# Performance work log

Hardware: AMD Instinct MI355X
Metric: run time of the kernel (lower is better)

Reference implementation:

```python
import jax, jax.numpy as jnp
import numpy as np

HEADS = 4
HIDDEN = 128
NEG_SLOPE = 0.2
BN_EPS = 1e-5


def setup_inputs() -> dict:
    key = jax.random.key(0)
    ks = jax.random.split(key, 10)
    N, E, C, H = 10000, 320000, HIDDEN, HEADS
    D = C  # out_channels per head == hidden_channels
    glorot = lambda k, shape, fan: jax.random.normal(k, shape, dtype=jnp.float32) * np.float32(np.sqrt(2.0 / fan))
    x = jax.random.normal(ks[0], (N, C), dtype=jnp.float32)
    edge_index = jax.random.randint(ks[1], (2, E), 0, N, dtype=jnp.int64)
    W_l = glorot(ks[2], (C, H * D), C + H * D)
    b_l = jnp.zeros((H * D,), dtype=jnp.float32)
    W_r = glorot(ks[3], (C, H * D), C + H * D)
    b_r = jnp.zeros((H * D,), dtype=jnp.float32)
    att = glorot(ks[4], (H, D), D)
    bias = jnp.zeros((D,), dtype=jnp.float32)
    gamma = jnp.ones((D,), dtype=jnp.float32)
    beta = jnp.zeros((D,), dtype=jnp.float32)
    return {"x": x, "edge_index": edge_index, "W_l": W_l, "b_l": b_l,
            "W_r": W_r, "b_r": b_r, "att": att, "bias": bias,
            "gamma": gamma, "beta": beta}


def reference(x, edge_index, W_l, b_l, W_r, b_r, att, bias, gamma, beta):
    N, C = x.shape
    H = HEADS
    D = C
    # add self loops (PyG default add_self_loops=True)
    loops = jnp.arange(N, dtype=edge_index.dtype)
    src = jnp.concatenate([edge_index[0], loops])  # [E+N]
    dst = jnp.concatenate([edge_index[1], loops])  # [E+N]
    # GATv2: separate source/target transforms (share_weights=False)
    xl = (x @ W_l + b_l).reshape(N, H, D)  # source-side features
    xr = (x @ W_r + b_r).reshape(N, H, D)  # target-side features
    # per-edge score: a^T LeakyReLU(xl_j + xr_i)
    m = jax.nn.leaky_relu(xl[src] + xr[dst], negative_slope=NEG_SLOPE)  # [E',H,D]
    e = jnp.einsum('ehd,hd->eh', m, att)  # [E',H]
    # segment softmax over destination nodes
    emax = jax.ops.segment_max(e, dst, num_segments=N)  # [N,H]
    ee = jnp.exp(e - emax[dst])
    denom = jax.ops.segment_sum(ee, dst, num_segments=N)  # [N,H]
    alpha = ee / (denom[dst] + 1e-16)  # [E',H]
    # aggregate: sum_j alpha_ij * xl_j
    out = jax.ops.segment_sum(alpha[..., None] * xl[src], dst, num_segments=N)  # [N,H,D]
    out = out.mean(axis=1) + bias  # concat=False -> mean over heads, then bias
    # BatchNorm1d (training-mode batch statistics) + ReLU; dropout p=0
    mu = out.mean(axis=0)
    var = out.var(axis=0)
    out = gamma * (out - mu) * jax.lax.rsqrt(var + BN_EPS) + beta
    return jax.nn.relu(out)
```

## Files before the change

kernel.cpp:

```cpp
#include <hip/hip_runtime.h>
#include <math.h>

#define HEADS 4
#define HD 512
#define NEG 0.2f
#define CAP 96
#define BNB 64

typedef __attribute__((ext_vector_type(8))) short bf16x8;
typedef __attribute__((ext_vector_type(4))) float f32x4;

__device__ __forceinline__ unsigned short f2b(float f) {
    unsigned u = __float_as_uint(f);
    unsigned r = (u + 0x7fff + ((u >> 16) & 1)) >> 16;
    return (unsigned short)r;
}
__device__ __forceinline__ unsigned pack2(float a, float b) {
    return (unsigned)f2b(a) | ((unsigned)f2b(b) << 16);
}
__device__ __forceinline__ float lo16(unsigned u) { return __uint_as_float(u << 16); }
__device__ __forceinline__ float hi16(unsigned u) { return __uint_as_float(u & 0xffff0000u); }

template<int CTRL>
__device__ __forceinline__ float dpp_mov(float v) {
    int x = __builtin_amdgcn_mov_dpp(__float_as_int(v), CTRL, 0xF, 0xF, true);
    return __int_as_float(x);
}
__device__ __forceinline__ float rowsum16(float s) {
    s += dpp_mov<0xB1>(s);
    s += dpp_mov<0x4E>(s);
    s += dpp_mov<0x124>(s);
    s += dpp_mov<0x128>(s);
    return s;
}

__global__ __launch_bounds__(256) void prologue1(
    const float* __restrict__ Wl, const float* __restrict__ Wr,
    unsigned short* __restrict__ wlt, unsigned short* __restrict__ wrt,
    const float* __restrict__ x, unsigned short* __restrict__ xb, int n8,
    const int* __restrict__ ei, int E, int* __restrict__ deg,
    int* __restrict__ adjf, int cvtxBlocks)
{
    const int bid = blockIdx.x;
    const int tid = threadIdx.x;
    if (bid < 128) {
        __shared__ float t[32][33];
        const int bx = bid & 15, by = (bid >> 4) & 3, bz = bid >> 6;
        const float* W = bz ? Wr : Wl;
        unsigned short* Wt = bz ? wrt : wlt;
        const int c0 = bx * 32, k0 = by * 32;
        {
            int k = tid >> 3, c4 = (tid & 7) * 4;
            float4 v = *(const float4*)(W + (size_t)(k0 + k) * 512 + c0 + c4);
            t[k][c4] = v.x; t[k][c4 + 1] = v.y; t[k][c4 + 2] = v.z; t[k][c4 + 3] = v.w;
        }
        __syncthreads();
        {
            int c = tid >> 3, k4 = (tid & 7) * 4;
            ushort4 o;
            o.x = f2b(t[k4][c]); o.y = f2b(t[k4 + 1][c]);
            o.z = f2b(t[k4 + 2][c]); o.w = f2b(t[k4 + 3][c]);
            *(ushort4*)(Wt + (size_t)(c0 + c) * 128 + k0 + k4) = o;
        }
    } else if (bid < 128 + cvtxBlocks) {
        int i = (bid - 128) * 256 + tid;
        if (i < n8) {
            const float4* px = (const float4*)(x + (size_t)i * 8);
            float4 f0 = px[0], f1 = px[1];
            uint4 u;
            u.x = pack2(f0.x, f0.y); u.y = pack2(f0.z, f0.w);
            u.z = pack2(f1.x, f1.y); u.w = pack2(f1.z, f1.w);
            ((uint4*)xb)[i] = u;
        }
    } else {
        int e = (bid - 128 - cvtxBlocks) * 256 + tid;
        if (e < E) {
            int src = ei[e], dst = ei[E + e];
            int pos = atomicAdd(&deg[dst], 1);
            if (pos < CAP) adjf[(size_t)dst * CAP + pos] = src;
        }
    }
}

__global__ __launch_bounds__(256) void prologue2(
    const unsigned short* __restrict__ xb,
    const unsigned short* __restrict__ wlt, const unsigned short* __restrict__ wrt,
    const float* __restrict__ bl, const float* __restrict__ br,
    unsigned short* __restrict__ xlb, unsigned short* __restrict__ xrb, int N)
{
    __shared__ float tile[4][16][132];

    const int bx = blockIdx.x, by = blockIdx.y;
    const int wv = threadIdx.x >> 6;
    const int lane = threadIdx.x & 63;
    const int wsel = by >> 2;
    const int cb0 = (by & 3) * 128;
    const unsigned short* Wt = wsel ? wrt : wlt;
    const float* bias = wsel ? br : bl;
    unsigned short* out = wsel ? xrb : xlb;

    const int r0 = bx * 64 + wv * 16;
    const int row16 = lane & 15;
    const int kg = lane >> 4;
    int ar = r0 + row16;
    int arc = (ar < N) ? ar : (N - 1);
    const unsigned short* xrow = xb + (size_t)arc * 128;

    f32x4 acc[8];
    #pragma unroll
    for (int i = 0; i < 8; ++i) acc[i] = (f32x4){0.f, 0.f, 0.f, 0.f};

    #pragma unroll
    for (int ks = 0; ks < 4; ++ks) {
        bf16x8 a = *(const bf16x8*)(xrow + ks * 32 + kg * 8);
        #pragma unroll
        for (int cb = 0; cb < 8; ++cb) {
            int col = cb0 + cb * 16 + row16;
            bf16x8 b = *(const bf16x8*)(Wt + (size_t)col * 128 + ks * 32 + kg * 8);
            acc[cb] = __builtin_amdgcn_mfma_f32_16x16x32_bf16(a, b, acc[cb], 0, 0, 0);
        }
    }

    #pragma unroll
    for (int cb = 0; cb < 8; ++cb) {
        int c = cb * 16 + row16;
        #pragma unroll
        for (int r = 0; r < 4; ++r)
            tile[wv][kg * 4 + r][c] = acc[cb][r];
    }
    __syncthreads();

    #pragma unroll
    for (int p = 0; p < 4; ++p) {
        int row = p * 4 + (lane >> 4);
        int grow = r0 + row;
        if (grow < N) {
            int c8 = (lane & 15) * 8;
            float4 b0v = *(const float4*)(bias + cb0 + c8);
            float4 b1v = *(const float4*)(bias + cb0 + c8 + 4);
            const float* tp = &tile[wv][row][c8];
            uint4 u;
            u.x = pack2(tp[0] + b0v.x, tp[1] + b0v.y);
            u.y = pack2(tp[2] + b0v.z, tp[3] + b0v.w);
            u.z = pack2(tp[4] + b1v.x, tp[5] + b1v.y);
            u.w = pack2(tp[6] + b1v.z, tp[7] + b1v.w);
            *(uint4*)(out + (size_t)grow * 512 + cb0 + c8) = u;
        }
    }
}

__global__ __launch_bounds__(256) void gat_aggr(
    const unsigned short* __restrict__ xlb, const unsigned short* __restrict__ xrb,
    const float* __restrict__ att, const float* __restrict__ bias,
    const int* __restrict__ degc, const int* __restrict__ adjf,
    float* __restrict__ outm, int N)
{
    const int wv = threadIdx.x >> 6;
    const int dst = blockIdx.x * 4 + wv;
    const int lane = threadIdx.x & 63;
    if (dst >= N) return;
    const int off = lane * 8;

    uint4 ur = *(const uint4*)(xrb + (size_t)dst * HD + off);
    float xrv[8] = {lo16(ur.x), hi16(ur.x), lo16(ur.y), hi16(ur.y),
                    lo16(ur.z), hi16(ur.z), lo16(ur.w), hi16(ur.w)};
    const float4* pa = (const float4*)(att + off);
    float4 a0 = pa[0], a1 = pa[1];
    float av[8]  = {a0.x, a0.y, a0.z, a0.w, a1.x, a1.y, a1.z, a1.w};

    float dsum0 = 0.f, dsum1 = 0.f;
    float acc0[8] = {0.f,0.f,0.f,0.f,0.f,0.f,0.f,0.f};
    float acc1[8] = {0.f,0.f,0.f,0.f,0.f,0.f,0.f,0.f};

    auto proc = [&](int src, float& dsum, float* acc) {
        uint4 u = *(const uint4*)(xlb + (size_t)src * HD + off);
        float xlv[8] = {lo16(u.x), hi16(u.x), lo16(u.y), hi16(u.y),
                        lo16(u.z), hi16(u.z), lo16(u.w), hi16(u.w)};
        float s = 0.f;
        #pragma unroll
        for (int j = 0; j < 8; ++j) {
            float v = xlv[j] + xrv[j];
            s = fmaf(fmaxf(v, NEG * v), av[j], s);
        }
        s = rowsum16(s);
        float p = __expf(s);
        dsum += p;
        #pragma unroll
        for (int j = 0; j < 8; ++j) acc[j] = fmaf(p, xlv[j], acc[j]);
    };

    const int* myadj = adjf + (size_t)dst * CAP;
    int dcount = min(degc[dst], CAP);

    proc(dst, dsum0, acc0);
    int i = 0;
    for (; i + 1 < dcount; i += 2) {
        int sA = myadj[i], sB = myadj[i + 1];
        proc(sA, dsum0, acc0);
        proc(sB, dsum1, acc1);
    }
    if (i < dcount) proc(myadj[i], dsum1, acc1);

    float inv = 1.f / (dsum0 + dsum1 + 1e-16f);
    float vv[8];
    #pragma unroll
    for (int j = 0; j < 8; ++j) {
        float v = (acc0[j] + acc1[j]) * inv;
        v += __shfl_xor(v, 16, 64);
        v += __shfl_xor(v, 32, 64);
        vv[j] = v;
    }
    if (lane < 16) {
        const float4* pb = (const float4*)(bias + lane * 8);
        float4 b0v = pb[0], b1v = pb[1];
        float4 o0 = make_float4(0.25f * vv[0] + b0v.x, 0.25f * vv[1] + b0v.y,
                                0.25f * vv[2] + b0v.z, 0.25f * vv[3] + b0v.w);
        float4 o1 = make_float4(0.25f * vv[4] + b1v.x, 0.25f * vv[5] + b1v.y,
                                0.25f * vv[6] + b1v.z, 0.25f * vv[7] + b1v.w);
        float4* po = (float4*)(outm + (size_t)dst * 128 + lane * 8);
        po[0] = o0; po[1] = o1;
    }
}

__global__ __launch_bounds__(256) void bn_stats(
    const float* __restrict__ outm, float* __restrict__ part1,
    float* __restrict__ part2, int N)
{
    const int t = threadIdx.x;
    const int c4 = t & 31, r = t >> 5;
    const int G = N >> 3;
    float4 s1 = make_float4(0.f, 0.f, 0.f, 0.f);
    float4 s2 = make_float4(0.f, 0.f, 0.f, 0.f);
    for (int g = blockIdx.x; g < G; g += BNB) {
        int row = g * 8 + r;
        float4 v = ((const float4*)outm)[(size_t)row * 32 + c4];
        s1.x += v.x; s1.y += v.y; s1.z += v.z; s1.w += v.w;
        s2.x = fmaf(v.x, v.x, s2.x); s2.y = fmaf(v.y, v.y, s2.y);
        s2.z = fmaf(v.z, v.z, s2.z); s2.w = fmaf(v.w, v.w, s2.w);
    }
    __shared__ float4 sh1[8][32], sh2[8][32];
    sh1[r][c4] = s1; sh2[r][c4] = s2;
    __syncthreads();
    if (r == 0) {
        #pragma unroll
        for (int w = 1; w < 8; ++w) {
            float4 x1 = sh1[w][c4], x2 = sh2[w][c4];
            s1.x += x1.x; s1.y += x1.y; s1.z += x1.z; s1.w += x1.w;
            s2.x += x2.x; s2.y += x2.y; s2.z += x2.z; s2.w += x2.w;
        }
        ((float4*)(part1 + (size_t)blockIdx.x * 128))[c4] = s1;
        ((float4*)(part2 + (size_t)blockIdx.x * 128))[c4] = s2;
    }
}

__global__ __launch_bounds__(128) void bn_reduce(
    const float* __restrict__ part1, const float* __restrict__ part2,
    const float* __restrict__ gamma, const float* __restrict__ beta,
    float* __restrict__ scale, float* __restrict__ shift, int N)
{
    const int t = threadIdx.x;
    const int c4 = t & 31, g = t >> 5;
    float4 s1 = make_float4(0.f, 0.f, 0.f, 0.f);
    float4 s2 = make_float4(0.f, 0.f, 0.f, 0.f);
    for (int b = g; b < BNB; b += 4) {
        float4 x1 = ((const float4*)(part1 + (size_t)b * 128))[c4];
        float4 x2 = ((const float4*)(part2 + (size_t)b * 128))[c4];
        s1.x += x1.x; s1.y += x1.y; s1.z += x1.z; s1.w += x1.w;
        s2.x += x2.x; s2.y += x2.y; s2.z += x2.z; s2.w += x2.w;
    }
    __shared__ float4 sh1[4][32], sh2[4][32];
    sh1[g][c4] = s1; sh2[g][c4] = s2;
    __syncthreads();
    if (g == 0) {
        #pragma unroll
        for (int w = 1; w < 4; ++w) {
            float4 x1 = sh1[w][c4], x2 = sh2[w][c4];
            s1.x += x1.x; s1.y += x1.y; s1.z += x1.z; s1.w += x1.w;
            s2.x += x2.x; s2.y += x2.y; s2.z += x2.z; s2.w += x2.w;
        }
        float inv_n = 1.0f / (float)N;
        float4 g4 = ((const float4*)gamma)[c4];
        float4 b4 = ((const float4*)beta)[c4];
        float4 sc, sf;
        float mu, var;
        mu = s1.x * inv_n; var = s2.x * inv_n - mu * mu;
        sc.x = g4.x * rsqrtf(var + 1e-5f); sf.x = b4.x - mu * sc.x;
        mu = s1.y * inv_n; var = s2.y * inv_n - mu * mu;
        sc.y = g4.y * rsqrtf(var + 1e-5f); sf.y = b4.y - mu * sc.y;
        mu = s1.z * inv_n; var = s2.z * inv_n - mu * mu;
        sc.z = g4.z * rsqrtf(var + 1e-5f); sf.z = b4.z - mu * sc.z;
        mu = s1.w * inv_n; var = s2.w * inv_n - mu * mu;
        sc.w = g4.w * rsqrtf(var + 1e-5f); sf.w = b4.w - mu * sc.w;
        ((float4*)scale)[c4] = sc;
        ((float4*)shift)[c4] = sf;
    }
}

__global__ __launch_bounds__(256) void finalize_b(
    float* __restrict__ outm, const float* __restrict__ scale,
    const float* __restrict__ shift, int N)
{
    int id = blockIdx.x * 256 + threadIdx.x;
    if (id >= N * 32) return;
    int d4 = (id & 31) * 4;
    float4 sc = *(const float4*)(scale + d4);
    float4 sh = *(const float4*)(shift + d4);
    float4 v = ((const float4*)outm)[id];
    float o;
    o = fmaf(v.x, sc.x, sh.x); v.x = o > 0.f ? o : 0.f;
    o = fmaf(v.y, sc.y, sh.y); v.y = o > 0.f ? o : 0.f;
    o = fmaf(v.z, sc.z, sh.z); v.z = o > 0.f ? o : 0.f;
    o = fmaf(v.w, sc.w, sh.w); v.w = o > 0.f ? o : 0.f;
    ((float4*)outm)[id] = v;
}

extern "C" void kernel_launch(void* const* d_in, const int* in_sizes, int n_in,
                              void* d_out, int out_size, void* d_ws, size_t ws_size,
                              hipStream_t stream) {
    const float* x     = (const float*)d_in[0];
    const int*   ei    = (const int*)d_in[1];
    const float* Wl    = (const float*)d_in[2];
    const float* bl    = (const float*)d_in[3];
    const float* Wr    = (const float*)d_in[4];
    const float* br    = (const float*)d_in[5];
    const float* att   = (const float*)d_in[6];
    const float* bias  = (const float*)d_in[7];
    const float* gamma = (const float*)d_in[8];
    const float* beta  = (const float*)d_in[9];

    const int N = in_sizes[0] / 128;
    const int E = in_sizes[1] / 2;

    unsigned short* xlb = (unsigned short*)d_ws;
    unsigned short* xrb = xlb + (size_t)N * 512;
    unsigned short* xb  = xrb + (size_t)N * 512;
    unsigned short* wlt = xb + (size_t)N * 128;
    unsigned short* wrt = wlt + 65536;
    int*   deg      = (int*)(wrt + 65536);
    int*   adjf     = deg + N;
    float* part1    = (float*)(adjf + (size_t)N * CAP);
    float* part2    = part1 + BNB * 128;
    float* scale    = part2 + BNB * 128;
    float* shift    = scale + 128;
    float* outm     = (float*)d_out;

    hipMemsetAsync(deg, 0, (size_t)N * sizeof(int), stream);

    int n8 = N * 128 / 8;
    int cvtxBlocks = (n8 + 255) / 256;
    int degBlocks = (E + 255) / 256;
    prologue1<<<128 + cvtxBlocks + degBlocks, 256, 0, stream>>>(
        Wl, Wr, wlt, wrt, x, xb, n8, ei, E, deg, adjf, cvtxBlocks);

    int nrb = (N + 63) / 64;
    dim3 gg(nrb, 8);
    prologue2<<<gg, 256, 0, stream>>>(xb, wlt, wrt, bl, br, xlb, xrb, N);

    gat_aggr<<<(N + 3) / 4, 256, 0, stream>>>(xlb, xrb, att, bias, deg, adjf, outm, N);

    bn_stats<<<BNB, 256, 0, stream>>>(outm, part1, part2, N);
    bn_reduce<<<1, 128, 0, stream>>>(part1, part2, gamma, beta, scale, shift, N);
    finalize_b<<<(N * 32 + 255) / 256, 256, 0, stream>>>(outm, scale, shift, N);
}
```

Before: 127.6 us.

## Split each destination's edges across four waves and fuse BN reduce into finalize

The aggregation kernel now gives each destination node a whole block, with its four waves each handling a quarter of the neighbor list. Partial sums go into shared memory and wave 0 combines them. Separately, the single-block bn_reduce kernel is removed: every finalize block recomputes scale and shift from the partial sums. This aims to shorten the per-node serial chain and cut one launch, at the cost of four times as many blocks, an extra barrier, and redundant reduction work in each finalize block.

```diff
diff --git a/kernel.cpp b/kernel.cpp
--- a/kernel.cpp
+++ b/kernel.cpp
@@ -155,11 +155,12 @@
     const int* __restrict__ degc, const int* __restrict__ adjf,
     float* __restrict__ outm, int N)
 {
+    const int dst = blockIdx.x;
     const int wv = threadIdx.x >> 6;
-    const int dst = blockIdx.x * 4 + wv;
     const int lane = threadIdx.x & 63;
-    if (dst >= N) return;
     const int off = lane * 8;
+
+    __shared__ float accs[4][64][9];
 
     uint4 ur = *(const uint4*)(xrb + (size_t)dst * HD + off);
     float xrv[8] = {lo16(ur.x), hi16(ur.x), lo16(ur.y), hi16(ur.y),
@@ -191,34 +192,52 @@
 
     const int* myadj = adjf + (size_t)dst * CAP;
     int dcount = min(degc[dst], CAP);
-
-    proc(dst, dsum0, acc0);
-    int i = 0;
-    for (; i + 1 < dcount; i += 2) {
+    int q = (dcount + 3) >> 2;
+    int b0 = min(wv * q, dcount);
+    int e0 = min((wv + 1) * q, dcount);
+
+    if (wv == 3) proc(dst, dsum0, acc0);
+    int i = b0;
+    for (; i + 1 < e0; i += 2) {
         int sA = myadj[i], sB = myadj[i + 1];
         proc(sA, dsum0, acc0);
         proc(sB, dsum1, acc1);
     }
-    if (i < dcount) proc(myadj[i], dsum1, acc1);
-
-    float inv = 1.f / (dsum0 + dsum1 + 1e-16f);
-    float vv[8];
-    #pragma unroll
-    for (int j = 0; j < 8; ++j) {
-        float v = (acc0[j] + acc1[j]) * inv;
-        v += __shfl_xor(v, 16, 64);
-        v += __shfl_xor(v, 32, 64);
-        vv[j] = v;
-    }
-    if (lane < 16) {
-        const float4* pb = (const float4*)(bias + lane * 8);
-        float4 b0v = pb[0], b1v = pb[1];
-        float4 o0 = make_float4(0.25f * vv[0] + b0v.x, 0.25f * vv[1] + b0v.y,
-                                0.25f * vv[2] + b0v.z, 0.25f * vv[3] + b0v.w);
-        float4 o1 = make_float4(0.25f * vv[4] + b1v.x, 0.25f * vv[5] + b1v.y,
-                                0.25f * vv[6] + b1v.z, 0.25f * vv[7] + b1v.w);
-        float4* po = (float4*)(outm + (size_t)dst * 128 + lane * 8);
-        po[0] = o0; po[1] = o1;
+    if (i < e0) proc(myadj[i], dsum1, acc1);
+
+    #pragma unroll
+    for (int j = 0; j < 8; ++j) accs[wv][lane][j] = acc0[j] + acc1[j];
+    accs[wv][lane][8] = dsum0 + dsum1;
+    __syncthreads();
+
+    if (wv == 0) {
+        float A[8] = {0.f, 0.f, 0.f, 0.f, 0.f, 0.f, 0.f, 0.f};
+        float D = 0.f;
+        #pragma unroll
+        for (int w = 0; w < 4; ++w) {
+            #pragma unroll
+            for (int j = 0; j < 8; ++j) A[j] += accs[w][lane][j];
+            D += accs[w][lane][8];
+        }
+        float inv = 1.f / (D + 1e-16f);
+        float vv[8];
+        #pragma unroll
+        for (int j = 0; j < 8; ++j) {
+            float v = A[j] * inv;
+            v += __shfl_xor(v, 16, 64);
+            v += __shfl_xor(v, 32, 64);
+            vv[j] = v;
+        }
+        if (lane < 16) {
+            const float4* pb = (const float4*)(bias + lane * 8);
+            float4 b0v = pb[0], b1v = pb[1];
+            float4 o0 = make_float4(0.25f * vv[0] + b0v.x, 0.25f * vv[1] + b0v.y,
+                                    0.25f * vv[2] + b0v.z, 0.25f * vv[3] + b0v.w);
+            float4 o1 = make_float4(0.25f * vv[4] + b1v.x, 0.25f * vv[5] + b1v.y,
+                                    0.25f * vv[6] + b1v.z, 0.25f * vv[7] + b1v.w);
+            float4* po = (float4*)(outm + (size_t)dst * 128 + lane * 8);
+            po[0] = o0; po[1] = o1;
+        }
     }
 }
 
@@ -253,27 +272,30 @@
     }
 }
 
-__global__ __launch_bounds__(128) void bn_reduce(
-    const float* __restrict__ part1, const float* __restrict__ part2,
-    const float* __restrict__ gamma, const float* __restrict__ beta,
-    float* __restrict__ scale, float* __restrict__ shift, int N)
+__global__ __launch_bounds__(256) void finalize_b(
+    float* __restrict__ outm, const float* __restrict__ part1,
+    const float* __restrict__ part2, const float* __restrict__ gamma,
+    const float* __restrict__ beta, int N)
 {
     const int t = threadIdx.x;
-    const int c4 = t & 31, g = t >> 5;
+    const int c4 = t & 31, r = t >> 5;
     float4 s1 = make_float4(0.f, 0.f, 0.f, 0.f);
     float4 s2 = make_float4(0.f, 0.f, 0.f, 0.f);
-    for (int b = g; b < BNB; b += 4) {
-        float4 x1 = ((const float4*)(part1 + (size_t)b * 128))[c4];
-        float4 x2 = ((const float4*)(part2 + (size_t)b * 128))[c4];
+    #pragma unroll
+    for (int b = 0; b < BNB / 8; ++b) {
+        int pb = r + b * 8;
+        float4 x1 = ((const float4*)(part1 + (size_t)pb * 128))[c4];
+        float4 x2 = ((const float4*)(part2 + (size_t)pb * 128))[c4];
         s1.x += x1.x; s1.y += x1.y; s1.z += x1.z; s1.w += x1.w;
         s2.x += x2.x; s2.y += x2.y; s2.z += x2.z; s2.w += x2.w;
     }
-    __shared__ float4 sh1[4][32], sh2[4][32];
-    sh1[g][c4] = s1; sh2[g][c4] = s2;
-    __syncthreads();
-    if (g == 0) {
-        #pragma unroll
-        for (int w = 1; w < 4; ++w) {
+    __shared__ float4 sh1[8][32], sh2[8][32];
+    __shared__ float4 ssc[32], ssh[32];
+    sh1[r][c4] = s1; sh2[r][c4] = s2;
+    __syncthreads();
+    if (r == 0) {
+        #pragma unroll
+        for (int w = 1; w < 8; ++w) {
             float4 x1 = sh1[w][c4], x2 = sh2[w][c4];
             s1.x += x1.x; s1.y += x1.y; s1.z += x1.z; s1.w += x1.w;
             s2.x += x2.x; s2.y += x2.y; s2.z += x2.z; s2.w += x2.w;
@@ -291,27 +313,21 @@
         sc.z = g4.z * rsqrtf(var + 1e-5f); sf.z = b4.z - mu * sc.z;
         mu = s1.w * inv_n; var = s2.w * inv_n - mu * mu;
         sc.w = g4.w * rsqrtf(var + 1e-5f); sf.w = b4.w - mu * sc.w;
-        ((float4*)scale)[c4] = sc;
-        ((float4*)shift)[c4] = sf;
-    }
-}
-
-__global__ __launch_bounds__(256) void finalize_b(
-    float* __restrict__ outm, const float* __restrict__ scale,
-    const float* __restrict__ shift, int N)
-{
-    int id = blockIdx.x * 256 + threadIdx.x;
-    if (id >= N * 32) return;
-    int d4 = (id & 31) * 4;
-    float4 sc = *(const float4*)(scale + d4);
-    float4 sh = *(const float4*)(shift + d4);
-    float4 v = ((const float4*)outm)[id];
-    float o;
-    o = fmaf(v.x, sc.x, sh.x); v.x = o > 0.f ? o : 0.f;
-    o = fmaf(v.y, sc.y, sh.y); v.y = o > 0.f ? o : 0.f;
-    o = fmaf(v.z, sc.z, sh.z); v.z = o > 0.f ? o : 0.f;
-    o = fmaf(v.w, sc.w, sh.w); v.w = o > 0.f ? o : 0.f;
-    ((float4*)outm)[id] = v;
+        ssc[c4] = sc; ssh[c4] = sf;
+    }
+    __syncthreads();
+
+    int id = blockIdx.x * 256 + t;
+    if (id < N * 32) {
+        float4 sc = ssc[c4], sh = ssh[c4];
+        float4 v = ((const float4*)outm)[id];
+        float o;
+        o = fmaf(v.x, sc.x, sh.x); v.x = o > 0.f ? o : 0.f;
+        o = fmaf(v.y, sc.y, sh.y); v.y = o > 0.f ? o : 0.f;
+        o = fmaf(v.z, sc.z, sh.z); v.z = o > 0.f ? o : 0.f;
+        o = fmaf(v.w, sc.w, sh.w); v.w = o > 0.f ? o : 0.f;
+        ((float4*)outm)[id] = v;
+    }
 }
 
 extern "C" void kernel_launch(void* const* d_in, const int* in_sizes, int n_in,
@@ -340,8 +356,6 @@
     int*   adjf     = deg + N;
     float* part1    = (float*)(adjf + (size_t)N * CAP);
     float* part2    = part1 + BNB * 128;
-    float* scale    = part2 + BNB * 128;
-    float* shift    = scale + 128;
     float* outm     = (float*)d_out;
 
     hipMemsetAsync(deg, 0, (size_t)N * sizeof(int), stream);
@@ -356,9 +370,8 @@
     dim3 gg(nrb, 8);
     prologue2<<<gg, 256, 0, stream>>>(xb, wlt, wrt, bl, br, xlb, xrb, N);
 
-    gat_aggr<<<(N + 3) / 4, 256, 0, stream>>>(xlb, xrb, att, bias, deg, adjf, outm, N);
+    gat_aggr<<<N, 256, 0, stream>>>(xlb, xrb, att, bias, deg, adjf, outm, N);
 
     bn_stats<<<BNB, 256, 0, stream>>>(outm, part1, part2, N);
-    bn_reduce<<<1, 128, 0, stream>>>(part1, part2, gamma, beta, scale, shift, N);
-    finalize_b<<<(N * 32 + 255) / 256, 256, 0, stream>>>(outm, scale, shift, N);
-}
+    finalize_b<<<(N * 32 + 255) / 256, 256, 0, stream>>>(outm, part1, part2, gamma, beta, N);
+}
```

New measurement: 121.6 us. -4.7%, faster.
